# Optimization experiments

Measured on AMD Instinct MI355X. Metric: run time of the kernel, lower is better.

Reference implementation:

```python
import jax, jax.numpy as jnp
import numpy as np

B, S, D, H = 2, 2048, 768, 12
DK = D // H


def setup_inputs() -> dict:
    key = jax.random.key(0)
    ks = jax.random.split(key, 13)
    s = 0.02
    return {
        "query": jax.random.normal(ks[0], (B, S, D), jnp.float32),
        "key": jax.random.normal(ks[1], (B, S, D), jnp.float32),
        "mask": jax.random.randint(ks[2], (B, S, S), 0, 2, jnp.int32),
        "short": jax.random.normal(ks[3], (B, H, S, S), jnp.float32),
        "aspect": jax.random.normal(ks[4], (B, D), jnp.float32),
        "Wq": jax.random.normal(ks[5], (D, D), jnp.float32) * s,
        "bq": jax.random.normal(ks[6], (D,), jnp.float32) * s,
        "Wk": jax.random.normal(ks[7], (D, D), jnp.float32) * s,
        "bk": jax.random.normal(ks[8], (D,), jnp.float32) * s,
        "Wd": jax.random.normal(ks[9], (D, DK), jnp.float32) * s,
        "bd": jax.random.normal(ks[10], (DK,), jnp.float32) * s,
        "weight_m": jax.random.normal(ks[11], (H, DK, DK), jnp.float32) * s,
        "bias_m": jax.random.normal(ks[12], (1,), jnp.float32) * s,
    }


def reference(query, key, mask, short, aspect, Wq, bq, Wk, bk, Wd, bd, weight_m, bias_m):
    b, sq, d = query.shape
    h, dk = weight_m.shape[0], weight_m.shape[1]
    # projections -> [B, H, S, DK]
    q = (query @ Wq + bq).reshape(b, sq, h, dk).transpose(0, 2, 1, 3)
    k = (key @ Wk + bk).reshape(b, -1, h, dk).transpose(0, 2, 1, 3)
    scores = jnp.einsum("bhsd,bhtd->bhst", q, k) / jnp.sqrt(jnp.float32(dk))
    # aspect path: same per-head vector broadcast over query positions
    a = aspect @ Wd + bd                                  # [B, DK]
    am = jnp.einsum("bd,hde->bhe", a, weight_m)           # [B, H, DK]
    aspect_scores = jnp.tanh(
        jnp.einsum("bhe,bhte->bht", am, k)[:, :, None, :] + bias_m
    )                                                      # [B, H, 1, S] broadcasts over s
    scores = scores + aspect_scores
    m = mask[:, :, :sq][:, None, :, :]                     # [B, 1, S, S]
    scores = jnp.where(m == 0, jnp.float32(-1e9), scores)
    scores = scores + short
    return jax.nn.softmax(scores, axis=-1)
```

## Files before the change

### kernel.cpp

```cpp
#include <hip/hip_runtime.h>
#include <math.h>

#define BB 2
#define SS 2048
#define DD 768
#define HH 12
#define DKK 64
#define BH (BB*HH)

typedef __attribute__((ext_vector_type(8))) __bf16 bf16x8;
typedef __attribute__((ext_vector_type(4))) float floatx4;
typedef unsigned short ushort_t;

__device__ inline float bf2f(ushort_t u) {
    unsigned int x = ((unsigned int)u) << 16;
    return __builtin_bit_cast(float, x);
}
__device__ inline ushort_t f2bf(float f) {
    unsigned int x = __builtin_bit_cast(unsigned int, f);
    unsigned int lsb = (x >> 16) & 1u;
    x += 0x7fffu + lsb;
    return (ushort_t)(x >> 16);
}

template<int ISBF>
__device__ inline float ldf(const void* p, size_t i) {
    if (ISBF) return bf2f(((const ushort_t*)p)[i]);
    else      return ((const float*)p)[i];
}

__global__ void detect_dtype(const ushort_t* __restrict__ q, int* __restrict__ flag) {
    __shared__ int cnt;
    if (threadIdx.x == 0) cnt = 0;
    __syncthreads();
    ushort_t u = q[2 * threadIdx.x];
    int e = (u >> 7) & 0xFF;
    if (e >= 0x66 && e <= 0x84) atomicAdd(&cnt, 1);
    __syncthreads();
    if (threadIdx.x == 0) *flag = (cnt >= 128) ? 1 : 0;
}

template<int ISBF>
__device__ void transpose_body(const void* __restrict__ in, ushort_t* __restrict__ out) {
    int t = blockIdx.x * 256 + threadIdx.x;
    if (t >= DD * DD) return;
    int e = t / DD, d = t - e * DD;
    out[t] = f2bf(ldf<ISBF>(in, (size_t)d * DD + e));
}
__global__ void transpose_w(const void* in, ushort_t* out, const int* flag) {
    if (*flag) transpose_body<1>(in, out); else transpose_body<0>(in, out);
}

template<int ISBF>
__device__ void gemm_body(const void* __restrict__ A, const ushort_t* __restrict__ Wt,
                          const void* __restrict__ bias, ushort_t* __restrict__ outp,
                          ushort_t* lAs, ushort_t* lBs)
{
    const int tid = threadIdx.x;
    const int lane = tid & 63, wave = tid >> 6;
    const int quad = lane >> 4, l15 = lane & 15;
    const int wm = wave >> 1, wn = wave & 1;
    const int r0 = blockIdx.y * 128;
    const int n0 = blockIdx.x * 128;

    floatx4 acc[4][4];
    #pragma unroll
    for (int m = 0; m < 4; m++)
        #pragma unroll
        for (int n = 0; n < 4; n++) acc[m][n] = (floatx4){0.f, 0.f, 0.f, 0.f};

    for (int kb = 0; kb < DD / 64; ++kb) {
        const int k0 = kb * 64;
        __syncthreads();
        #pragma unroll
        for (int i = 0; i < 4; i++) {
            int idx = tid + i * 256;
            int r = idx >> 3, c = idx & 7;
            int gc = c ^ (r & 7);
            size_t aoff = (size_t)(r0 + r) * DD + k0 + gc * 8;
            bf16x8 va;
            if (ISBF) {
                va = *(const bf16x8*)((const ushort_t*)A + aoff);
            } else {
                const float* Af = (const float*)A;
                floatx4 f0 = *(const floatx4*)(Af + aoff);
                floatx4 f1 = *(const floatx4*)(Af + aoff + 4);
                union { ushort_t u[8]; bf16x8 v; } t;
                #pragma unroll
                for (int j = 0; j < 4; j++) { t.u[j] = f2bf(f0[j]); t.u[4 + j] = f2bf(f1[j]); }
                va = t.v;
            }
            *(bf16x8*)(lAs + r * 64 + c * 8) = va;
            bf16x8 vb = *(const bf16x8*)(Wt + (size_t)(n0 + r) * DD + k0 + gc * 8);
            *(bf16x8*)(lBs + r * 64 + c * 8) = vb;
        }
        __syncthreads();
        #pragma unroll
        for (int kc = 0; kc < 2; kc++) {
            bf16x8 af[4], bfr[4];
            #pragma unroll
            for (int m = 0; m < 4; m++) {
                int row = wm * 64 + m * 16 + l15;
                int chunk = (kc * 4 + quad) ^ (row & 7);
                af[m] = *(const bf16x8*)(lAs + row * 64 + chunk * 8);
            }
            #pragma unroll
            for (int n = 0; n < 4; n++) {
                int row = wn * 64 + n * 16 + l15;
                int chunk = (kc * 4 + quad) ^ (row & 7);
                bfr[n] = *(const bf16x8*)(lBs + row * 64 + chunk * 8);
            }
            #pragma unroll
            for (int m = 0; m < 4; m++)
                #pragma unroll
                for (int n = 0; n < 4; n++)
                    acc[m][n] = __builtin_amdgcn_mfma_f32_16x16x32_bf16(af[m], bfr[n], acc[m][n], 0, 0, 0);
        }
    }
    #pragma unroll
    for (int n = 0; n < 4; n++) {
        int E = n0 + wn * 64 + n * 16 + l15;
        float bv = ldf<ISBF>(bias, E);
        int h = E >> 6, dk = E & 63;
        #pragma unroll
        for (int m = 0; m < 4; m++) {
            #pragma unroll
            for (int j = 0; j < 4; j++) {
                int R = r0 + wm * 64 + m * 16 + quad * 4 + j;
                int b = R >> 11, s = R & 2047;
                float v = acc[m][n][j] + bv;
                outp[(((size_t)(b * HH + h)) * SS + s) * DKK + dk] = f2bf(v);
            }
        }
    }
}
__global__ __launch_bounds__(256, 2) void gemm_proj(
    const void* A, const ushort_t* Wt, const void* bias, ushort_t* outp, const int* flag)
{
    __shared__ __align__(16) ushort_t lAs[128 * 64];
    __shared__ __align__(16) ushort_t lBs[128 * 64];
    if (*flag) gemm_body<1>(A, Wt, bias, outp, lAs, lBs);
    else       gemm_body<0>(A, Wt, bias, outp, lAs, lBs);
}

template<int ISBF>
__device__ void aspect_body(const void* __restrict__ aspect, const void* __restrict__ Wd,
                            const void* __restrict__ bd, const void* __restrict__ wm,
                            float* __restrict__ am_out, float* a_sh)
{
    int tid = threadIdx.x;
    if (tid < BB * DKK) {
        int b = tid >> 6, dk = tid & 63;
        float s = 0.f;
        for (int d = 0; d < DD; ++d)
            s += ldf<ISBF>(aspect, b * DD + d) * ldf<ISBF>(Wd, (size_t)d * DKK + dk);
        s += ldf<ISBF>(bd, dk);
        a_sh[tid] = s;
    }
    __syncthreads();
    for (int idx = tid; idx < BB * HH * DKK; idx += 256) {
        int b = idx / (HH * DKK);
        int rem = idx - b * (HH * DKK);
        int h = rem >> 6, e = rem & 63;
        float s = 0.f;
        for (int dk = 0; dk < DKK; ++dk)
            s += a_sh[b * DKK + dk] * ldf<ISBF>(wm, (size_t)(h * DKK + dk) * DKK + e);
        am_out[idx] = s;
    }
}
__global__ void aspect_am(const void* aspect, const void* Wd, const void* bd,
                          const void* wm, float* am_out, const int* flag) {
    __shared__ float a_sh[BB * DKK];
    if (*flag) aspect_body<1>(aspect, Wd, bd, wm, am_out, a_sh);
    else       aspect_body<0>(aspect, Wd, bd, wm, am_out, a_sh);
}

template<int ISBF>
__device__ void ascore_body(const float* __restrict__ am, const ushort_t* __restrict__ kws,
                            const void* __restrict__ bias_m, float* __restrict__ asc) {
    int idx = blockIdx.x * 256 + threadIdx.x;
    if (idx >= BH * SS) return;
    int bh = idx >> 11;
    int t = idx & 2047;
    const float* amv = am + bh * DKK;
    const ushort_t* kp = kws + ((size_t)bh * SS + t) * DKK;
    float s = 0.f;
    #pragma unroll 8
    for (int e = 0; e < DKK; e++) s += amv[e] * bf2f(kp[e]);
    s += ldf<ISBF>(bias_m, 0);
    asc[idx] = tanhf(s);
}
__global__ void ascore_k(const float* am, const ushort_t* kws, const void* bias_m,
                         float* asc, const int* flag) {
    if (*flag) ascore_body<1>(am, kws, bias_m, asc);
    else       ascore_body<0>(am, kws, bias_m, asc);
}

template<int ISBF>
__device__ void scores_body(const ushort_t* __restrict__ qws, const ushort_t* __restrict__ kws,
                            const float* __restrict__ asc, const int* __restrict__ mask,
                            const void* __restrict__ shr, void* __restrict__ outv,
                            float (*red)[16])
{
    const int tid = threadIdx.x;
    const int lane = tid & 63, wave = tid >> 6;
    const int quad = lane >> 4, l15 = lane & 15;
    const int r0 = blockIdx.x * 16;
    const int bh = blockIdx.y;
    const int b = bh / HH;

    const ushort_t* qp = qws + ((size_t)bh * SS + r0) * DKK;
    const ushort_t* kp = kws + ((size_t)bh * SS) * DKK;

    bf16x8 aq0 = *(const bf16x8*)(qp + l15 * DKK + quad * 8);
    bf16x8 aq1 = *(const bf16x8*)(qp + l15 * DKK + 32 + quad * 8);

    const int c0 = wave * 128;
    floatx4 acc[8];
    #pragma unroll
    for (int i = 0; i < 8; i++) {
        const ushort_t* kt = kp + (size_t)(c0 + i * 16 + l15) * DKK + quad * 8;
        bf16x8 b0 = *(const bf16x8*)(kt);
        bf16x8 b1 = *(const bf16x8*)(kt + 32);
        floatx4 a = (floatx4){0.f, 0.f, 0.f, 0.f};
        a = __builtin_amdgcn_mfma_f32_16x16x32_bf16(aq0, b0, a, 0, 0, 0);
        a = __builtin_amdgcn_mfma_f32_16x16x32_bf16(aq1, b1, a, 0, 0, 0);
        acc[i] = a;
    }

    float mx[4] = {-3.0e38f, -3.0e38f, -3.0e38f, -3.0e38f};
    const float* ascp = asc + bh * SS;
    #pragma unroll
    for (int i = 0; i < 8; i++) {
        int ct = c0 + i * 16 + l15;
        float av = ascp[ct];
        #pragma unroll
        for (int j = 0; j < 4; j++) {
            int r = r0 + quad * 4 + j;
            int mk = mask[((size_t)(b * SS + r)) * SS + ct];
            float sv = ldf<ISBF>(shr, ((size_t)(bh * SS + r)) * SS + ct);
            float s = (mk == 0) ? -1e9f : (acc[i][j] * 0.125f + av);
            s += sv;
            acc[i][j] = s;
            mx[j] = fmaxf(mx[j], s);
        }
    }
    #pragma unroll
    for (int j = 0; j < 4; j++)
        #pragma unroll
        for (int off = 1; off < 16; off <<= 1)
            mx[j] = fmaxf(mx[j], __shfl_xor(mx[j], off));

    if (l15 == 0) {
        #pragma unroll
        for (int j = 0; j < 4; j++) red[wave][quad * 4 + j] = mx[j];
    }
    __syncthreads();
    float rmax[4];
    #pragma unroll
    for (int j = 0; j < 4; j++) {
        int row = quad * 4 + j;
        float m = red[0][row];
        #pragma unroll
        for (int w = 1; w < 16; w++) m = fmaxf(m, red[w][row]);
        rmax[j] = m;
    }
    __syncthreads();

    float sm[4] = {0.f, 0.f, 0.f, 0.f};
    #pragma unroll
    for (int i = 0; i < 8; i++)
        #pragma unroll
        for (int j = 0; j < 4; j++) {
            float p = __expf(acc[i][j] - rmax[j]);
            acc[i][j] = p;
            sm[j] += p;
        }
    #pragma unroll
    for (int j = 0; j < 4; j++)
        #pragma unroll
        for (int off = 1; off < 16; off <<= 1)
            sm[j] += __shfl_xor(sm[j], off);
    if (l15 == 0) {
        #pragma unroll
        for (int j = 0; j < 4; j++) red[wave][quad * 4 + j] = sm[j];
    }
    __syncthreads();
    float rinv[4];
    #pragma unroll
    for (int j = 0; j < 4; j++) {
        int row = quad * 4 + j;
        float s = red[0][row];
        #pragma unroll
        for (int w = 1; w < 16; w++) s += red[w][row];
        rinv[j] = 1.0f / s;
    }

    #pragma unroll
    for (int i = 0; i < 8; i++) {
        int ct = c0 + i * 16 + l15;
        #pragma unroll
        for (int j = 0; j < 4; j++) {
            int r = r0 + quad * 4 + j;
            size_t oidx = ((size_t)(bh * SS + r)) * SS + ct;
            float v = acc[i][j] * rinv[j];
            if (ISBF) ((ushort_t*)outv)[oidx] = f2bf(v);
            else      ((float*)outv)[oidx] = v;
        }
    }
}
__global__ __launch_bounds__(1024, 4) void scores_softmax(
    const ushort_t* qws, const ushort_t* kws, const float* asc, const int* mask,
    const void* shr, void* outv, const int* flag)
{
    __shared__ float red[16][16];
    if (*flag) scores_body<1>(qws, kws, asc, mask, shr, outv, red);
    else       scores_body<0>(qws, kws, asc, mask, shr, outv, red);
}

extern "C" void kernel_launch(void* const* d_in, const int* in_sizes, int n_in,
                              void* d_out, int out_size, void* d_ws, size_t ws_size,
                              hipStream_t stream) {
    const void* query  = d_in[0];
    const void* key    = d_in[1];
    const int*  mask   = (const int*)d_in[2];
    const void* shr    = d_in[3];
    const void* aspect = d_in[4];
    const void* Wq     = d_in[5];
    const void* bq     = d_in[6];
    const void* Wk     = d_in[7];
    const void* bk     = d_in[8];
    const void* Wd     = d_in[9];
    const void* bd     = d_in[10];
    const void* wm     = d_in[11];
    const void* bias_m = d_in[12];

    char* ws = (char*)d_ws;
    const size_t QK_BYTES = (size_t)BH * SS * DKK * 2;
    const size_t WT_BYTES = (size_t)DD * DD * 2;
    ushort_t* qws = (ushort_t*)(ws);
    ushort_t* kws = (ushort_t*)(ws + QK_BYTES);
    ushort_t* wtq = (ushort_t*)(ws + 2 * QK_BYTES);
    ushort_t* wtk = (ushort_t*)(ws + 2 * QK_BYTES + WT_BYTES);
    float*    amb = (float*)   (ws + 2 * QK_BYTES + 2 * WT_BYTES);
    float*    asc = (float*)   (ws + 2 * QK_BYTES + 2 * WT_BYTES + 8192);
    int*      flg = (int*)     (ws + 2 * QK_BYTES + 2 * WT_BYTES + 8192 + (size_t)BH * SS * 4);

    detect_dtype<<<1, 256, 0, stream>>>((const ushort_t*)query, flg);
    transpose_w<<<dim3((DD * DD + 255) / 256), 256, 0, stream>>>(Wq, wtq, flg);
    transpose_w<<<dim3((DD * DD + 255) / 256), 256, 0, stream>>>(Wk, wtk, flg);
    gemm_proj<<<dim3(DD / 128, (BB * SS) / 128), 256, 0, stream>>>(query, wtq, bq, qws, flg);
    gemm_proj<<<dim3(DD / 128, (BB * SS) / 128), 256, 0, stream>>>(key,   wtk, bk, kws, flg);
    aspect_am<<<1, 256, 0, stream>>>(aspect, Wd, bd, wm, amb, flg);
    ascore_k<<<dim3((BH * SS + 255) / 256), 256, 0, stream>>>(amb, kws, bias_m, asc, flg);
    scores_softmax<<<dim3(SS / 16, BH), 1024, 0, stream>>>(qws, kws, asc, mask, shr, d_out, flg);
}
```

Before: 929.6 us.

## Transpose MFMA operand order so each lane holds contiguous columns for vector loads

Swaps the A/B operands of the QK^T MFMA so the accumulator layout gives each lane four consecutive key columns of one query row. The mask, short, aspect-score loads and the output stores become 16-byte vector accesses instead of scalar strided ones, and the row reductions need only two cross-lane shuffles. The aspect-score kernel also loads K in 8-element vectors. The aim is to cut memory transactions in the bandwidth-bound softmax epilogue; the cost is a different reduction pattern that has to stay correct.

```diff
diff --git a/kernel.cpp b/kernel.cpp
--- a/kernel.cpp
+++ b/kernel.cpp
@@ -10,7 +10,9 @@
 
 typedef __attribute__((ext_vector_type(8))) __bf16 bf16x8;
 typedef __attribute__((ext_vector_type(4))) float floatx4;
+typedef __attribute__((ext_vector_type(4))) int intx4;
 typedef unsigned short ushort_t;
+typedef __attribute__((ext_vector_type(4))) unsigned short ushortx4;
 
 __device__ inline float bf2f(ushort_t u) {
     unsigned int x = ((unsigned int)u) << 16;
@@ -185,8 +187,13 @@
     const float* amv = am + bh * DKK;
     const ushort_t* kp = kws + ((size_t)bh * SS + t) * DKK;
     float s = 0.f;
-    #pragma unroll 8
-    for (int e = 0; e < DKK; e++) s += amv[e] * bf2f(kp[e]);
+    #pragma unroll
+    for (int e0 = 0; e0 < DKK; e0 += 8) {
+        union { bf16x8 v; ushort_t u[8]; } t8;
+        t8.v = *(const bf16x8*)(kp + e0);
+        #pragma unroll
+        for (int j = 0; j < 8; j++) s += amv[e0 + j] * bf2f(t8.u[j]);
+    }
     s += ldf<ISBF>(bias_m, 0);
     asc[idx] = tanhf(s);
 }
@@ -212,100 +219,90 @@
     const ushort_t* qp = qws + ((size_t)bh * SS + r0) * DKK;
     const ushort_t* kp = kws + ((size_t)bh * SS) * DKK;
 
-    bf16x8 aq0 = *(const bf16x8*)(qp + l15 * DKK + quad * 8);
-    bf16x8 aq1 = *(const bf16x8*)(qp + l15 * DKK + 32 + quad * 8);
+    bf16x8 bq0 = *(const bf16x8*)(qp + l15 * DKK + quad * 8);
+    bf16x8 bq1 = *(const bf16x8*)(qp + l15 * DKK + 32 + quad * 8);
 
     const int c0 = wave * 128;
     floatx4 acc[8];
     #pragma unroll
     for (int i = 0; i < 8; i++) {
         const ushort_t* kt = kp + (size_t)(c0 + i * 16 + l15) * DKK + quad * 8;
-        bf16x8 b0 = *(const bf16x8*)(kt);
-        bf16x8 b1 = *(const bf16x8*)(kt + 32);
+        bf16x8 a0 = *(const bf16x8*)(kt);
+        bf16x8 a1 = *(const bf16x8*)(kt + 32);
         floatx4 a = (floatx4){0.f, 0.f, 0.f, 0.f};
-        a = __builtin_amdgcn_mfma_f32_16x16x32_bf16(aq0, b0, a, 0, 0, 0);
-        a = __builtin_amdgcn_mfma_f32_16x16x32_bf16(aq1, b1, a, 0, 0, 0);
+        a = __builtin_amdgcn_mfma_f32_16x16x32_bf16(a0, bq0, a, 0, 0, 0);
+        a = __builtin_amdgcn_mfma_f32_16x16x32_bf16(a1, bq1, a, 0, 0, 0);
         acc[i] = a;
     }
 
-    float mx[4] = {-3.0e38f, -3.0e38f, -3.0e38f, -3.0e38f};
-    const float* ascp = asc + bh * SS;
+    const int r = r0 + l15;
+    const float* ascp  = asc + (size_t)bh * SS;
+    const int*   maskp = mask + ((size_t)(b * SS + r)) * SS;
+    const size_t rowoff = ((size_t)(bh * SS + r)) * SS;
+
+    float mx = -3.0e38f;
     #pragma unroll
     for (int i = 0; i < 8; i++) {
-        int ct = c0 + i * 16 + l15;
-        float av = ascp[ct];
+        int ct = c0 + i * 16 + quad * 4;
+        floatx4 av = *(const floatx4*)(ascp + ct);
+        intx4   mk = *(const intx4*)(maskp + ct);
+        floatx4 sv;
+        if (ISBF) {
+            ushortx4 s4 = *(const ushortx4*)((const ushort_t*)shr + rowoff + ct);
+            #pragma unroll
+            for (int j = 0; j < 4; j++) sv[j] = bf2f(s4[j]);
+        } else {
+            sv = *(const floatx4*)((const float*)shr + rowoff + ct);
+        }
         #pragma unroll
         for (int j = 0; j < 4; j++) {
-            int r = r0 + quad * 4 + j;
-            int mk = mask[((size_t)(b * SS + r)) * SS + ct];
-            float sv = ldf<ISBF>(shr, ((size_t)(bh * SS + r)) * SS + ct);
-            float s = (mk == 0) ? -1e9f : (acc[i][j] * 0.125f + av);
-            s += sv;
+            float s = (mk[j] == 0) ? -1e9f : (acc[i][j] * 0.125f + av[j]);
+            s += sv[j];
             acc[i][j] = s;
-            mx[j] = fmaxf(mx[j], s);
-        }
-    }
-    #pragma unroll
-    for (int j = 0; j < 4; j++)
-        #pragma unroll
-        for (int off = 1; off < 16; off <<= 1)
-            mx[j] = fmaxf(mx[j], __shfl_xor(mx[j], off));
-
-    if (l15 == 0) {
-        #pragma unroll
-        for (int j = 0; j < 4; j++) red[wave][quad * 4 + j] = mx[j];
-    }
-    __syncthreads();
-    float rmax[4];
-    #pragma unroll
-    for (int j = 0; j < 4; j++) {
-        int row = quad * 4 + j;
-        float m = red[0][row];
-        #pragma unroll
-        for (int w = 1; w < 16; w++) m = fmaxf(m, red[w][row]);
-        rmax[j] = m;
-    }
-    __syncthreads();
-
-    float sm[4] = {0.f, 0.f, 0.f, 0.f};
+            mx = fmaxf(mx, s);
+        }
+    }
+    mx = fmaxf(mx, __shfl_xor(mx, 16));
+    mx = fmaxf(mx, __shfl_xor(mx, 32));
+    if (lane < 16) red[wave][lane] = mx;
+    __syncthreads();
+    float rmax = red[0][l15];
+    #pragma unroll
+    for (int w = 1; w < 16; w++) rmax = fmaxf(rmax, red[w][l15]);
+    __syncthreads();
+
+    float sm = 0.f;
     #pragma unroll
     for (int i = 0; i < 8; i++)
         #pragma unroll
         for (int j = 0; j < 4; j++) {
-            float p = __expf(acc[i][j] - rmax[j]);
+            float p = __expf(acc[i][j] - rmax);
             acc[i][j] = p;
-            sm[j] += p;
-        }
-    #pragma unroll
-    for (int j = 0; j < 4; j++)
-        #pragma unroll
-        for (int off = 1; off < 16; off <<= 1)
-            sm[j] += __shfl_xor(sm[j], off);
-    if (l15 == 0) {
-        #pragma unroll
-        for (int j = 0; j < 4; j++) red[wave][quad * 4 + j] = sm[j];
-    }
-    __syncthreads();
-    float rinv[4];
-    #pragma unroll
-    for (int j = 0; j < 4; j++) {
-        int row = quad * 4 + j;
-        float s = red[0][row];
-        #pragma unroll
-        for (int w = 1; w < 16; w++) s += red[w][row];
-        rinv[j] = 1.0f / s;
-    }
+            sm += p;
+        }
+    sm += __shfl_xor(sm, 16);
+    sm += __shfl_xor(sm, 32);
+    if (lane < 16) red[wave][lane] = sm;
+    __syncthreads();
+    float tot = red[0][l15];
+    #pragma unroll
+    for (int w = 1; w < 16; w++) tot += red[w][l15];
+    float rinv = 1.0f / tot;
 
     #pragma unroll
     for (int i = 0; i < 8; i++) {
-        int ct = c0 + i * 16 + l15;
-        #pragma unroll
-        for (int j = 0; j < 4; j++) {
-            int r = r0 + quad * 4 + j;
-            size_t oidx = ((size_t)(bh * SS + r)) * SS + ct;
-            float v = acc[i][j] * rinv[j];
-            if (ISBF) ((ushort_t*)outv)[oidx] = f2bf(v);
-            else      ((float*)outv)[oidx] = v;
+        int ct = c0 + i * 16 + quad * 4;
+        size_t oidx = rowoff + ct;
+        if (ISBF) {
+            ushortx4 o4;
+            #pragma unroll
+            for (int j = 0; j < 4; j++) o4[j] = f2bf(acc[i][j] * rinv);
+            *(ushortx4*)((ushort_t*)outv + oidx) = o4;
+        } else {
+            floatx4 o4;
+            #pragma unroll
+            for (int j = 0; j < 4; j++) o4[j] = acc[i][j] * rinv;
+            *(floatx4*)((float*)outv + oidx) = o4;
         }
     }
 }
```

New measurement: 959.5 us. +3.2%, slower.
